# Optimization experiments

Hardware: AMD Instinct MI355X
Metric: run time of the kernel (lower is better)

The kernel has to match this reference:

```python
import jax, jax.numpy as jnp
import numpy as np

NUM_TOKENS = 8192
CODEBOOK_DIM = 64
BETA = 0.25
DECAY = 0.99
EPS = 1e-05
B, C, H, W = 32, 64, 32, 32


def setup_inputs() -> dict:
    key = jax.random.key(0)
    k1, k2, k3, k4 = jax.random.split(key, 4)
    z = jax.random.normal(k1, (B, C, H, W), dtype=jnp.float32)
    emb = jax.random.normal(k2, (NUM_TOKENS, CODEBOOK_DIM), dtype=jnp.float32)
    ema_w = jax.random.normal(k3, (NUM_TOKENS, CODEBOOK_DIM), dtype=jnp.float32)
    cluster_size = jax.random.uniform(k4, (NUM_TOKENS,), dtype=jnp.float32)
    return {"z": z, "emb": emb, "ema_w": ema_w, "cluster_size": cluster_size}


def reference(z, emb, ema_w, cluster_size):
    # NCHW -> NHWC, flatten to [N, D]
    z_nhwc = jnp.transpose(z, (0, 2, 3, 1))
    z_flat = z_nhwc.reshape(-1, CODEBOOK_DIM)  # [N, D]

    # squared distances: ||z||^2 + ||e||^2 - 2 z e^T  -> [N, K]
    d = (jnp.sum(z_flat * z_flat, axis=1, keepdims=True)
         + jnp.sum(emb * emb, axis=1)
         - 2.0 * jnp.einsum('nd,kd->nk', z_flat, emb))
    idx = jnp.argmin(d, axis=1)  # [N] int

    z_q = emb[idx].reshape(z_nhwc.shape)  # gather + reshape

    # EMA updates (training-mode buffer math); one-hot matmuls expressed as segment sums
    new_cluster = jax.ops.segment_sum(jnp.ones_like(idx, dtype=z.dtype), idx, num_segments=NUM_TOKENS)
    cs = DECAY * cluster_size + (1.0 - DECAY) * new_cluster
    new_ema_w = jax.ops.segment_sum(z_flat, idx, num_segments=NUM_TOKENS)
    ema_w_out = DECAY * ema_w + (1.0 - DECAY) * new_ema_w
    cs_sum = jnp.sum(cs)
    cs_norm = (cs + EPS) / (cs_sum + NUM_TOKENS * EPS)
    emb_out = ema_w_out / cs_norm[:, None]

    # commitment loss uses z_q from the OLD codebook (as in torch code)
    loss = BETA * jnp.mean((jax.lax.stop_gradient(z_q) - z_nhwc) ** 2)

    # straight-through estimator, back to NCHW
    z_q_st = z_nhwc + jax.lax.stop_gradient(z_q - z_nhwc)
    z_q_st = jnp.transpose(z_q_st, (0, 3, 1, 2))
    return z_q_st, loss, idx, cs_norm, ema_w_out, emb_out
```

## Files before the change

kernel.cpp:

```cpp
#include <hip/hip_runtime.h>
#include <float.h>

#define N_TOK   32768
#define DIM     64
#define K_CODES 8192
#define HWSZ    1024
#define CHW     65536
#define NELEM   2097152

typedef short  bf16x8 __attribute__((ext_vector_type(8)));
typedef float  f32x16 __attribute__((ext_vector_type(16)));

static __device__ __forceinline__ unsigned short f2bf(float x) {
    unsigned u = __float_as_uint(x);
    unsigned r = u + 0x7FFFu + ((u >> 16) & 1u);
    return (unsigned short)(r >> 16);
}
static __device__ __forceinline__ float bf2f(unsigned short h) {
    return __uint_as_float(((unsigned)h) << 16);
}

__global__ __launch_bounds__(256) void prep_e(const float* __restrict__ emb,
                                              const float* __restrict__ ema_w,
                                              const float* __restrict__ csize,
                                              unsigned short* __restrict__ blob,
                                              float* __restrict__ eng,
                                              unsigned long long* __restrict__ packed,
                                              int* __restrict__ cnt_i,
                                              float* __restrict__ sums,
                                              float* __restrict__ emao_out) {
    __shared__ float part[512];
    __shared__ float csp[4];
    const int gid = blockIdx.x * 256 + threadIdx.x;
    packed[gid] = ~0ull;
    if (gid < K_CODES) cnt_i[gid] = 0;
    if (gid == 1) sums[1] = 0.f;

    #pragma unroll
    for (int j = 0; j < 16; ++j) {
        int i = gid + j * 32768;
        emao_out[i] = 0.99f * ema_w[i];
    }

    if (blockIdx.x == 0) {
        float s = 0.f;
        #pragma unroll
        for (int j = 0; j < 32; ++j) s += csize[threadIdx.x * 32 + j];
        #pragma unroll
        for (int m = 32; m >= 1; m >>= 1) s += __shfl_xor(s, m, 64);
        if ((threadIdx.x & 63) == 0) csp[threadIdx.x >> 6] = s;
        __syncthreads();
        if (threadIdx.x == 0) sums[0] = csp[0] + csp[1] + csp[2] + csp[3];
    }

    int tile = blockIdx.x;
    #pragma unroll
    for (int u0 = 0; u0 < 2; ++u0) {
        int u = threadIdx.x + u0 * 256;
        int s = u >> 7, h = (u >> 6) & 1, n = u & 63;
        const float* src = emb + (tile * 64 + n) * 64 + s * 16 + h * 8;
        float4 v0 = *(const float4*)src;
        float4 v1 = *(const float4*)(src + 4);
        float x[8] = {v0.x, v0.y, v0.z, v0.w, v1.x, v1.y, v1.z, v1.w};
        unsigned short hi[8], lo[8];
        float ss = 0.f;
        #pragma unroll
        for (int j = 0; j < 8; ++j) {
            hi[j] = f2bf(x[j]);
            lo[j] = f2bf(x[j] - bf2f(hi[j]));
            ss += x[j] * x[j];
        }
        part[u] = ss;
        unsigned short* dhi = blob + (size_t)tile * 8192 + ((s * 2 + 0) * 2 + h) * 512 + n * 8;
        unsigned short* dlo = blob + (size_t)tile * 8192 + ((s * 2 + 1) * 2 + h) * 512 + n * 8;
        uint4 ph, pl;
        ph.x = (unsigned)hi[0] | ((unsigned)hi[1] << 16);
        ph.y = (unsigned)hi[2] | ((unsigned)hi[3] << 16);
        ph.z = (unsigned)hi[4] | ((unsigned)hi[5] << 16);
        ph.w = (unsigned)hi[6] | ((unsigned)hi[7] << 16);
        pl.x = (unsigned)lo[0] | ((unsigned)lo[1] << 16);
        pl.y = (unsigned)lo[2] | ((unsigned)lo[3] << 16);
        pl.z = (unsigned)lo[4] | ((unsigned)lo[5] << 16);
        pl.w = (unsigned)lo[6] | ((unsigned)lo[7] << 16);
        *(uint4*)dhi = ph;
        *(uint4*)dlo = pl;
    }
    __syncthreads();
    if (threadIdx.x < 64) {
        float s = 0.f;
        #pragma unroll
        for (int j = 0; j < 8; ++j) s += part[threadIdx.x + j * 64];
        eng[tile * 64 + threadIdx.x] = s;
    }
}

__global__ __launch_bounds__(256, 3) void vq_argmin(const float* __restrict__ z,
                                                    const unsigned short* __restrict__ blob,
                                                    const float* __restrict__ eng,
                                                    unsigned long long* __restrict__ packed) {
    __shared__ __align__(16) unsigned short zh[64 * 72];
    __shared__ __align__(16) unsigned short zl[64 * 72];
    __shared__ unsigned long long red[64 * 4];

    const int tid  = threadIdx.x;
    const int lane = tid & 63;
    const int wid  = tid >> 6;
    const int l31  = lane & 31, h = lane >> 5;

    const int tb = blockIdx.x & 511;
    const int ks = blockIdx.x >> 9;
    const int n0 = tb * 64;
    const int zbase = (n0 >> 10) * CHW + (n0 & 1023);

    {
        int f4 = tid & 15;
        int c0 = tid >> 4;
        #pragma unroll
        for (int r = 0; r < 4; ++r) {
            int c = c0 * 4 + r;
            float4 v = *(const float4*)(z + zbase + c * HWSZ + f4 * 4);
            float x[4] = {v.x, v.y, v.z, v.w};
            #pragma unroll
            for (int e = 0; e < 4; ++e) {
                int t = f4 * 4 + e;
                float xs = -2.0f * x[e];
                unsigned short hi = f2bf(xs);
                zh[t * 72 + c] = hi;
                zl[t * 72 + c] = f2bf(xs - bf2f(hi));
            }
        }
    }
    __syncthreads();

    bf16x8 T0h[4], T0l[4], T1h[4], T1l[4];
    {
        int r0 = l31;
        int r1 = 32 + l31;
        #pragma unroll
        for (int s = 0; s < 4; ++s) {
            T0h[s] = *(const bf16x8*)(&zh[r0 * 72 + s * 16 + h * 8]);
            T0l[s] = *(const bf16x8*)(&zl[r0 * 72 + s * 16 + h * 8]);
            T1h[s] = *(const bf16x8*)(&zh[r1 * 72 + s * 16 + h * 8]);
            T1l[s] = *(const bf16x8*)(&zl[r1 * 72 + s * 16 + h * 8]);
        }
    }

    const int hk0 = ks * 64 + wid;
    const unsigned short* bp = blob + (size_t)(hk0 >> 1) * 8192 + ((hk0 & 1) * 32 + l31) * 8;
    const float* ep = eng + (hk0 >> 1) * 64 + (hk0 & 1) * 32 + 4 * h;
    int scode = __builtin_amdgcn_readfirstlane((hk0 >> 1) * 64 + (hk0 & 1) * 32);

    bf16x8 Eh[4], El[4];
    #pragma unroll
    for (int s = 0; s < 4; ++s) {
        Eh[s] = *(const bf16x8*)(bp + (4 * s + h) * 512);
        El[s] = *(const bf16x8*)(bp + (4 * s + 2 + h) * 512);
    }
    float4 g0 = *(const float4*)(ep);
    float4 g1 = *(const float4*)(ep + 8);
    float4 g2 = *(const float4*)(ep + 16);
    float4 g3 = *(const float4*)(ep + 24);

    float minv0 = FLT_MAX, minv1 = FLT_MAX;
    int   mini0 = 0,       mini1 = 0;

    for (int i = 0; i < 16; ++i) {
        f32x16 ac0, ac1;
        ac0[0]  = g0.x; ac0[1]  = g0.y; ac0[2]  = g0.z; ac0[3]  = g0.w;
        ac0[4]  = g1.x; ac0[5]  = g1.y; ac0[6]  = g1.z; ac0[7]  = g1.w;
        ac0[8]  = g2.x; ac0[9]  = g2.y; ac0[10] = g2.z; ac0[11] = g2.w;
        ac0[12] = g3.x; ac0[13] = g3.y; ac0[14] = g3.z; ac0[15] = g3.w;
        ac1 = ac0;

        ep += 128;
        g0 = *(const float4*)(ep);
        g1 = *(const float4*)(ep + 8);
        g2 = *(const float4*)(ep + 16);
        g3 = *(const float4*)(ep + 24);

        __builtin_amdgcn_s_setprio(1);
        #pragma unroll
        for (int s = 0; s < 4; ++s) {
            ac0 = __builtin_amdgcn_mfma_f32_32x32x16_bf16(El[s], T0h[s], ac0, 0, 0, 0);
            ac1 = __builtin_amdgcn_mfma_f32_32x32x16_bf16(El[s], T1h[s], ac1, 0, 0, 0);
            ac0 = __builtin_amdgcn_mfma_f32_32x32x16_bf16(Eh[s], T0l[s], ac0, 0, 0, 0);
            ac1 = __builtin_amdgcn_mfma_f32_32x32x16_bf16(Eh[s], T1l[s], ac1, 0, 0, 0);
            ac0 = __builtin_amdgcn_mfma_f32_32x32x16_bf16(Eh[s], T0h[s], ac0, 0, 0, 0);
            ac1 = __builtin_amdgcn_mfma_f32_32x32x16_bf16(Eh[s], T1h[s], ac1, 0, 0, 0);
        }
        __builtin_amdgcn_s_setprio(0);

        bp += 2 * 8192;
        #pragma unroll
        for (int s = 0; s < 4; ++s) {
            Eh[s] = *(const bf16x8*)(bp + (4 * s + h) * 512);
            El[s] = *(const bf16x8*)(bp + (4 * s + 2 + h) * 512);
        }

        #pragma unroll
        for (int r = 0; r < 16; ++r) {
            int code = scode + ((r & 3) + 8 * (r >> 2));
            if (ac0[r] < minv0) { minv0 = ac0[r]; mini0 = code; }
            if (ac1[r] < minv1) { minv1 = ac1[r]; mini1 = code; }
        }
        scode += 128;
    }
    mini0 += 4 * h;
    mini1 += 4 * h;

    unsigned u0 = __float_as_uint(minv0);
    u0 = (u0 & 0x80000000u) ? ~u0 : (u0 | 0x80000000u);
    unsigned long long k0 = ((unsigned long long)u0 << 32) | (unsigned)mini0;
    unsigned u1 = __float_as_uint(minv1);
    u1 = (u1 & 0x80000000u) ? ~u1 : (u1 | 0x80000000u);
    unsigned long long k1 = ((unsigned long long)u1 << 32) | (unsigned)mini1;
    unsigned long long o0 = __shfl_xor(k0, 32, 64);
    if (o0 < k0) k0 = o0;
    unsigned long long o1 = __shfl_xor(k1, 32, 64);
    if (o1 < k1) k1 = o1;
    if (h == 0) {
        red[l31 * 4 + wid]        = k0;
        red[(32 + l31) * 4 + wid] = k1;
    }
    __syncthreads();
    if (tid < 64) {
        unsigned long long a = red[tid * 4], b = red[tid * 4 + 1];
        unsigned long long c = red[tid * 4 + 2], d = red[tid * 4 + 3];
        unsigned long long m = (b < a) ? b : a;
        if (c < m) m = c;
        if (d < m) m = d;
        atomicMin(&packed[n0 + tid], m);
    }
}

__global__ __launch_bounds__(256) void zq_loss(const float* __restrict__ z,
                                               const float* __restrict__ emb,
                                               const unsigned long long* __restrict__ packed,
                                               float* __restrict__ zq_out,
                                               float* __restrict__ idx_out,
                                               int* __restrict__ idx_i32,
                                               int* __restrict__ cnt_i,
                                               float* __restrict__ loss_sum,
                                               float* __restrict__ emao_out) {
    __shared__ float e_lds[64][68];
    __shared__ float z_lds[64][68];

    const int tid = threadIdx.x;
    const int n0  = blockIdx.x * 64;
    const int t   = tid >> 2, q = tid & 3;
    const int n   = n0 + t;
    const int w   = tid >> 6, lane = tid & 63;
    const int b   = n0 >> 10;
    const int hw0 = n0 & 1023;
    const int zb  = b * CHW + hw0;

    const int idx = (int)(packed[n] & 0xFFFFFFFFull);
    if (q == 0) {
        idx_out[n] = (float)idx;
        idx_i32[n] = idx;
        atomicAdd(&cnt_i[idx], 1);
    }
    {
        const float* er = emb + idx * 64 + q * 16;
        float4 e0 = *(const float4*)er,       e1 = *(const float4*)(er + 4);
        float4 e2 = *(const float4*)(er + 8), e3 = *(const float4*)(er + 12);
        *(float4*)&e_lds[t][q * 16]      = e0;
        *(float4*)&e_lds[t][q * 16 + 4]  = e1;
        *(float4*)&e_lds[t][q * 16 + 8]  = e2;
        *(float4*)&e_lds[t][q * 16 + 12] = e3;
    }
    {
        const int f4 = tid & 15, c0 = tid >> 4;
        #pragma unroll
        for (int r = 0; r < 4; ++r) {
            int c = c0 * 4 + r;
            float4 v = *(const float4*)(z + zb + c * HWSZ + f4 * 4);
            z_lds[f4 * 4 + 0][c] = v.x;
            z_lds[f4 * 4 + 1][c] = v.y;
            z_lds[f4 * 4 + 2][c] = v.z;
            z_lds[f4 * 4 + 3][c] = v.w;
        }
    }
    __syncthreads();

    #pragma unroll
    for (int u = 0; u < 16; ++u) {
        int tt = w * 16 + u;
        int ix = __shfl(idx, u * 4, 64);
        atomicAdd(&emao_out[ix * 64 + lane], 0.01f * z_lds[tt][lane]);
    }

    {
        const int f4 = tid & 15, c0 = tid >> 4;
        #pragma unroll
        for (int r = 0; r < 4; ++r) {
            int c = c0 * 4 + r;
            float4 o;
            { float zv = z_lds[f4*4+0][c]; o.x = zv + (e_lds[f4*4+0][c] - zv); }
            { float zv = z_lds[f4*4+1][c]; o.y = zv + (e_lds[f4*4+1][c] - zv); }
            { float zv = z_lds[f4*4+2][c]; o.z = zv + (e_lds[f4*4+2][c] - zv); }
            { float zv = z_lds[f4*4+3][c]; o.w = zv + (e_lds[f4*4+3][c] - zv); }
            *(float4*)(zq_out + zb + c * HWSZ + f4 * 4) = o;
        }
    }
    float lsum = 0.f;
    #pragma unroll
    for (int j = 0; j < 16; ++j) {
        int c = q * 16 + j;
        float dd = e_lds[t][c] - z_lds[t][c];
        lsum += dd * dd;
    }
    #pragma unroll
    for (int m = 32; m >= 1; m >>= 1) lsum += __shfl_xor(lsum, m, 64);
    if ((tid & 63) == 0) atomicAdd(loss_sum, lsum);
}

__global__ __launch_bounds__(256) void norm_div(const int* __restrict__ cnt_i,
                                                const float* __restrict__ csize,
                                                const float* __restrict__ sums,
                                                const float* __restrict__ emao_out,
                                                float* __restrict__ csn_out,
                                                float* __restrict__ loss_out,
                                                float* __restrict__ embo_out) {
    const int g = blockIdx.x * 256 + threadIdx.x;
    const int c = g >> 6;
    const float denom = 0.99f * sums[0] + 0.01f * (float)N_TOK + (float)(K_CODES * 1e-5);
    const float cv  = 0.99f * csize[c] + 0.01f * (float)cnt_i[c];
    const float csn = (cv + 1e-5f) / denom;
    if ((g & 63) == 0) csn_out[c] = csn;
    embo_out[g] = emao_out[g] / csn;
    if (g == 0) *loss_out = 0.25f * sums[1] * (1.0f / (float)NELEM);
}

extern "C" void kernel_launch(void* const* d_in, const int* in_sizes, int n_in,
                              void* d_out, int out_size, void* d_ws, size_t ws_size,
                              hipStream_t stream) {
    (void)in_sizes; (void)n_in; (void)out_size; (void)ws_size;
    const float* z     = (const float*)d_in[0];
    const float* emb   = (const float*)d_in[1];
    const float* ema_w = (const float*)d_in[2];
    const float* csize = (const float*)d_in[3];

    float* out      = (float*)d_out;
    float* zq_out   = out;
    float* loss_out = out + 2097152;
    float* idx_out  = out + 2097153;
    float* csn_out  = out + 2129921;
    float* emao_out = out + 2138113;
    float* embo_out = out + 2662401;

    char* wsb = (char*)d_ws;
    unsigned short*     blob    = (unsigned short*)(wsb);
    float*              eng     = (float*)(wsb + 2097152);
    unsigned long long* packed  = (unsigned long long*)(wsb + 2129920);
    int*                idx_i32 = (int*)(wsb + 2392064);
    int*                cnt_i   = (int*)(wsb + 2523136);
    float*              sums    = (float*)(wsb + 2555904);

    prep_e<<<128, 256, 0, stream>>>(emb, ema_w, csize, blob, eng, packed, cnt_i,
                                    sums, emao_out);
    vq_argmin<<<2048, 256, 0, stream>>>(z, blob, eng, packed);
    zq_loss<<<N_TOK / 64, 256, 0, stream>>>(z, emb, packed, zq_out, idx_out,
                                            idx_i32, cnt_i, sums + 1, emao_out);
    norm_div<<<NELEM / 4 / 256, 256, 0, stream>>>(cnt_i, csize, sums, emao_out,
                                                  csn_out, loss_out, embo_out);
}
```

Baseline: 204.9 us.

## Fuse argmin and z_q/loss kernels via last-block tile counter, halve K splits

Merges the argmin kernel and the z_q/loss/EMA scatter kernel into one launch. Each token tile now splits the codebook into 2 halves instead of 4, so each block scans twice as many codes. The block that finishes a tile last, detected through an atomic tile counter, runs the gather, straight-through output, loss and EMA scatter for that tile. This removes one kernel launch and the reread of packed indices, at the cost of fewer blocks (less parallelism) and a serialized epilogue tail on the last-arriving blocks.

New measurement: 353.0 us. +72.3%, slower.

```diff
diff --git a/kernel.cpp b/kernel.cpp
--- a/kernel.cpp
+++ b/kernel.cpp
@@ -28,12 +28,14 @@
                                               unsigned long long* __restrict__ packed,
                                               int* __restrict__ cnt_i,
                                               float* __restrict__ sums,
-                                              float* __restrict__ emao_out) {
+                                              float* __restrict__ emao_out,
+                                              int* __restrict__ tile_ctr) {
     __shared__ float part[512];
     __shared__ float csp[4];
     const int gid = blockIdx.x * 256 + threadIdx.x;
     packed[gid] = ~0ull;
     if (gid < K_CODES) cnt_i[gid] = 0;
+    if (gid < 512) tile_ctr[gid] = 0;
     if (gid == 1) sums[1] = 0.f;
 
     #pragma unroll
@@ -94,13 +96,22 @@
     }
 }
 
-__global__ __launch_bounds__(256, 3) void vq_argmin(const float* __restrict__ z,
-                                                    const unsigned short* __restrict__ blob,
-                                                    const float* __restrict__ eng,
-                                                    unsigned long long* __restrict__ packed) {
-    __shared__ __align__(16) unsigned short zh[64 * 72];
-    __shared__ __align__(16) unsigned short zl[64 * 72];
-    __shared__ unsigned long long red[64 * 4];
+__global__ __launch_bounds__(256, 3) void vq_fused(const float* __restrict__ z,
+                                                   const unsigned short* __restrict__ blob,
+                                                   const float* __restrict__ eng,
+                                                   unsigned long long* __restrict__ packed,
+                                                   const float* __restrict__ emb,
+                                                   float* __restrict__ zq_out,
+                                                   float* __restrict__ idx_out,
+                                                   int* __restrict__ cnt_i,
+                                                   float* __restrict__ loss_sum,
+                                                   float* __restrict__ emao_out,
+                                                   int* __restrict__ tile_ctr) {
+    __shared__ __align__(16) char lds_raw[35072];
+    __shared__ int is_last;
+    unsigned short* zh = (unsigned short*)lds_raw;
+    unsigned short* zl = (unsigned short*)(lds_raw + 9216);
+    unsigned long long* red = (unsigned long long*)(lds_raw + 18432);
 
     const int tid  = threadIdx.x;
     const int lane = tid & 63;
@@ -145,7 +156,7 @@
         }
     }
 
-    const int hk0 = ks * 64 + wid;
+    const int hk0 = ks * 128 + wid;
     const unsigned short* bp = blob + (size_t)(hk0 >> 1) * 8192 + ((hk0 & 1) * 32 + l31) * 8;
     const float* ep = eng + (hk0 >> 1) * 64 + (hk0 & 1) * 32 + 4 * h;
     int scode = __builtin_amdgcn_readfirstlane((hk0 >> 1) * 64 + (hk0 & 1) * 32);
@@ -164,7 +175,7 @@
     float minv0 = FLT_MAX, minv1 = FLT_MAX;
     int   mini0 = 0,       mini1 = 0;
 
-    for (int i = 0; i < 16; ++i) {
+    for (int i = 0; i < 32; ++i) {
         f32x16 ac0, ac1;
         ac0[0]  = g0.x; ac0[1]  = g0.y; ac0[2]  = g0.z; ac0[3]  = g0.w;
         ac0[4]  = g1.x; ac0[5]  = g1.y; ac0[6]  = g1.z; ac0[7]  = g1.w;
@@ -231,83 +242,76 @@
         if (d < m) m = d;
         atomicMin(&packed[n0 + tid], m);
     }
-}
-
-__global__ __launch_bounds__(256) void zq_loss(const float* __restrict__ z,
-                                               const float* __restrict__ emb,
-                                               const unsigned long long* __restrict__ packed,
-                                               float* __restrict__ zq_out,
-                                               float* __restrict__ idx_out,
-                                               int* __restrict__ idx_i32,
-                                               int* __restrict__ cnt_i,
-                                               float* __restrict__ loss_sum,
-                                               float* __restrict__ emao_out) {
-    __shared__ float e_lds[64][68];
-    __shared__ float z_lds[64][68];
-
-    const int tid = threadIdx.x;
-    const int n0  = blockIdx.x * 64;
-    const int t   = tid >> 2, q = tid & 3;
-    const int n   = n0 + t;
-    const int w   = tid >> 6, lane = tid & 63;
-    const int b   = n0 >> 10;
-    const int hw0 = n0 & 1023;
-    const int zb  = b * CHW + hw0;
-
-    const int idx = (int)(packed[n] & 0xFFFFFFFFull);
-    if (q == 0) {
-        idx_out[n] = (float)idx;
-        idx_i32[n] = idx;
-        atomicAdd(&cnt_i[idx], 1);
-    }
-    {
-        const float* er = emb + idx * 64 + q * 16;
+
+    __threadfence();
+    __syncthreads();
+    if (tid == 0) is_last = (atomicAdd(&tile_ctr[tb], 1) == 1);
+    __syncthreads();
+    if (!is_last) return;
+    __threadfence();
+
+    float* e_lds  = (float*)lds_raw;
+    float* z_ldsf = (float*)(lds_raw + 17408);
+    int*   idx_s  = (int*)(lds_raw + 34816);
+
+    if (tid < 64) {
+        unsigned long long p = __hip_atomic_load(&packed[n0 + tid], __ATOMIC_RELAXED,
+                                                 __HIP_MEMORY_SCOPE_AGENT);
+        int ix = (int)(p & 0xFFFFFFFFull);
+        idx_s[tid] = ix;
+        idx_out[n0 + tid] = (float)ix;
+        atomicAdd(&cnt_i[ix], 1);
+    }
+    __syncthreads();
+
+    const int t = tid >> 2, q = tid & 3;
+    const int ixt = idx_s[t];
+    {
+        const float* er = emb + ixt * 64 + q * 16;
         float4 e0 = *(const float4*)er,       e1 = *(const float4*)(er + 4);
         float4 e2 = *(const float4*)(er + 8), e3 = *(const float4*)(er + 12);
-        *(float4*)&e_lds[t][q * 16]      = e0;
-        *(float4*)&e_lds[t][q * 16 + 4]  = e1;
-        *(float4*)&e_lds[t][q * 16 + 8]  = e2;
-        *(float4*)&e_lds[t][q * 16 + 12] = e3;
+        *(float4*)&e_lds[t * 68 + q * 16]      = e0;
+        *(float4*)&e_lds[t * 68 + q * 16 + 4]  = e1;
+        *(float4*)&e_lds[t * 68 + q * 16 + 8]  = e2;
+        *(float4*)&e_lds[t * 68 + q * 16 + 12] = e3;
     }
     {
         const int f4 = tid & 15, c0 = tid >> 4;
         #pragma unroll
         for (int r = 0; r < 4; ++r) {
             int c = c0 * 4 + r;
-            float4 v = *(const float4*)(z + zb + c * HWSZ + f4 * 4);
-            z_lds[f4 * 4 + 0][c] = v.x;
-            z_lds[f4 * 4 + 1][c] = v.y;
-            z_lds[f4 * 4 + 2][c] = v.z;
-            z_lds[f4 * 4 + 3][c] = v.w;
+            float4 v = *(const float4*)(z + zbase + c * HWSZ + f4 * 4);
+            z_ldsf[(f4 * 4 + 0) * 68 + c] = v.x;
+            z_ldsf[(f4 * 4 + 1) * 68 + c] = v.y;
+            z_ldsf[(f4 * 4 + 2) * 68 + c] = v.z;
+            z_ldsf[(f4 * 4 + 3) * 68 + c] = v.w;
         }
     }
     __syncthreads();
 
     #pragma unroll
     for (int u = 0; u < 16; ++u) {
-        int tt = w * 16 + u;
-        int ix = __shfl(idx, u * 4, 64);
-        atomicAdd(&emao_out[ix * 64 + lane], 0.01f * z_lds[tt][lane]);
-    }
-
+        int tt = wid * 16 + u;
+        atomicAdd(&emao_out[idx_s[tt] * 64 + lane], 0.01f * z_ldsf[tt * 68 + lane]);
+    }
     {
         const int f4 = tid & 15, c0 = tid >> 4;
         #pragma unroll
         for (int r = 0; r < 4; ++r) {
             int c = c0 * 4 + r;
             float4 o;
-            { float zv = z_lds[f4*4+0][c]; o.x = zv + (e_lds[f4*4+0][c] - zv); }
-            { float zv = z_lds[f4*4+1][c]; o.y = zv + (e_lds[f4*4+1][c] - zv); }
-            { float zv = z_lds[f4*4+2][c]; o.z = zv + (e_lds[f4*4+2][c] - zv); }
-            { float zv = z_lds[f4*4+3][c]; o.w = zv + (e_lds[f4*4+3][c] - zv); }
-            *(float4*)(zq_out + zb + c * HWSZ + f4 * 4) = o;
+            { float zv = z_ldsf[(f4*4+0)*68+c]; o.x = zv + (e_lds[(f4*4+0)*68+c] - zv); }
+            { float zv = z_ldsf[(f4*4+1)*68+c]; o.y = zv + (e_lds[(f4*4+1)*68+c] - zv); }
+            { float zv = z_ldsf[(f4*4+2)*68+c]; o.z = zv + (e_lds[(f4*4+2)*68+c] - zv); }
+            { float zv = z_ldsf[(f4*4+3)*68+c]; o.w = zv + (e_lds[(f4*4+3)*68+c] - zv); }
+            *(float4*)(zq_out + zbase + c * HWSZ + f4 * 4) = o;
         }
     }
     float lsum = 0.f;
     #pragma unroll
     for (int j = 0; j < 16; ++j) {
         int c = q * 16 + j;
-        float dd = e_lds[t][c] - z_lds[t][c];
+        float dd = e_lds[t * 68 + c] - z_ldsf[t * 68 + c];
         lsum += dd * dd;
     }
     #pragma unroll
@@ -350,18 +354,17 @@
     float* embo_out = out + 2662401;
 
     char* wsb = (char*)d_ws;
-    unsigned short*     blob    = (unsigned short*)(wsb);
-    float*              eng     = (float*)(wsb + 2097152);
-    unsigned long long* packed  = (unsigned long long*)(wsb + 2129920);
-    int*                idx_i32 = (int*)(wsb + 2392064);
-    int*                cnt_i   = (int*)(wsb + 2523136);
-    float*              sums    = (float*)(wsb + 2555904);
+    unsigned short*     blob     = (unsigned short*)(wsb);
+    float*              eng      = (float*)(wsb + 2097152);
+    unsigned long long* packed   = (unsigned long long*)(wsb + 2129920);
+    int*                tile_ctr = (int*)(wsb + 2392064);
+    int*                cnt_i    = (int*)(wsb + 2523136);
+    float*              sums     = (float*)(wsb + 2555904);
 
     prep_e<<<128, 256, 0, stream>>>(emb, ema_w, csize, blob, eng, packed, cnt_i,
-                                    sums, emao_out);
-    vq_argmin<<<2048, 256, 0, stream>>>(z, blob, eng, packed);
-    zq_loss<<<N_TOK / 64, 256, 0, stream>>>(z, emb, packed, zq_out, idx_out,
-                                            idx_i32, cnt_i, sums + 1, emao_out);
+                                    sums, emao_out, tile_ctr);
+    vq_fused<<<1024, 256, 0, stream>>>(z, blob, eng, packed, emb, zq_out, idx_out,
+                                       cnt_i, sums + 1, emao_out, tile_ctr);
     norm_div<<<NELEM / 4 / 256, 256, 0, stream>>>(cnt_i, csize, sums, emao_out,
                                                   csn_out, loss_out, embo_out);
 }
```
